# Optimization experiments

Measured on AMD Instinct MI355X. Metric: run time of the kernel, lower is better.

The kernel has to match this reference:

```python
import jax, jax.numpy as jnp
import numpy as np

N_ENTITIES = 4096
FEATURE_DIM = 512
CELLS = 39
PAIRS = 8192


def setup_inputs() -> dict:
    key = jax.random.key(0)
    k_emb, k_idx, k_wg, k_wl = jax.random.split(key, 4)
    embedding = jax.random.normal(k_emb, (N_ENTITIES, FEATURE_DIM), dtype=jnp.float32)
    index = jax.random.randint(k_idx, (CELLS, PAIRS, 2), 0, N_ENTITIES, dtype=jnp.int32)
    # kaiming_uniform-style scale for the global bilinear weight
    bound_g = np.sqrt(6.0 / FEATURE_DIM)
    weights_global = jax.random.uniform(k_wg, (FEATURE_DIM, FEATURE_DIM), minval=-bound_g, maxval=bound_g, dtype=jnp.float32)
    # per-cell diagonal scaling vectors (original stores them as [d,1] params)
    weights_local = jax.random.uniform(k_wl, (CELLS, FEATURE_DIM), minval=-bound_g, maxval=bound_g, dtype=jnp.float32)
    return {"embedding": embedding, "index": index,
            "weights_global": weights_global, "weights_local": weights_local}


def reference(embedding, index, weights_global, weights_local):
    # Original per-cell math: einsum('bn,nm,mj,jk,bk->b', A, diag(wl), W, diag(wl), B)
    # diag(wl) @ ... is just elementwise scaling of the gathered embeddings, so:
    #   out[c,p] = sum_{n,k} (A[c,p,n]*wl[c,n]) * W[n,k] * (B[c,p,k]*wl[c,k])
    wl = weights_local[:, None, :]                      # [C,1,d]
    A = embedding[index[..., 0]] * wl                   # [C,P,d]
    B = embedding[index[..., 1]] * wl                   # [C,P,d]
    return jnp.einsum('cpn,nk,cpk->cp', A, weights_global, B)  # [C,P]
```

## Files before the change

### kernel.cpp

```cpp
#include <hip/hip_runtime.h>
#include <stdint.h>

#define NE 4096
#define FD 512
#define NCELLS 39
#define NPAIRS 8192
#define NT (FD / 64)

typedef __attribute__((ext_vector_type(8))) short short8;
typedef __attribute__((ext_vector_type(8))) unsigned short ushort8;
typedef __attribute__((ext_vector_type(4))) float f32x4;
typedef __attribute__((ext_vector_type(4))) unsigned int uint4v;

__device__ __forceinline__ unsigned short f2bf(float f) {
  union { float f; uint32_t u; } v; v.f = f;
  uint32_t u = v.u;
  return (unsigned short)((u + 0x7fffu + ((u >> 16) & 1u)) >> 16);
}
__device__ __forceinline__ float bf2f(unsigned short b) {
  return __uint_as_float(((uint32_t)b) << 16);
}

__device__ __forceinline__ void async16(const void* g, void* l) {
  __builtin_amdgcn_global_load_lds((const __attribute__((address_space(1))) void*)g,
                                   (__attribute__((address_space(3))) void*)l, 16, 0, 0);
}

__global__ __launch_bounds__(256) void conv_e(const float* __restrict__ E,
                                              unsigned short* __restrict__ Ebf) {
  const int i = blockIdx.x * 256 + threadIdx.x;
  const float4 v = ((const float4*)E)[i];
  ushort4 o;
  o.x = f2bf(v.x); o.y = f2bf(v.y); o.z = f2bf(v.z); o.w = f2bf(v.w);
  ((ushort4*)Ebf)[i] = o;
}

__global__ __launch_bounds__(256) void prep_w(const float* __restrict__ W,
                                              const float* __restrict__ wl,
                                              unsigned short* __restrict__ Wt,
                                              int c0) {
  __shared__ float tile[32][33];
  const int ci = blockIdx.z;
  const int tn = blockIdx.x * 32, tk = blockIdx.y * 32;
  const int tx = threadIdx.x & 31, ty = threadIdx.x >> 5;
  const float* wlr = wl + (size_t)(c0 + ci) * FD;
#pragma unroll
  for (int i = 0; i < 4; i++) {
    int n = tn + ty + i * 8;
    tile[ty + i * 8][tx] = W[(size_t)n * FD + tk + tx] * wlr[n];
  }
  __syncthreads();
  unsigned short* dst = Wt + (size_t)ci * FD * FD;
#pragma unroll
  for (int i = 0; i < 4; i++) {
    int kout = tk + ty + i * 8;
    dst[(size_t)kout * FD + tn + tx] = f2bf(tile[tx][ty + i * 8] * wlr[kout]);
  }
}

__global__ __launch_bounds__(512, 2) void gemm_k(const unsigned short* __restrict__ Ebf,
                                                 const unsigned short* __restrict__ Wt,
                                                 unsigned short* __restrict__ U) {
  __shared__ unsigned short lds[2][2][2][128 * 64];
  const int t = threadIdx.x;
  const int id = blockIdx.x;
  const int xcd = id & 7;
  const int j = id >> 3;
  const int bxh = j & 1;
  const int by = (j >> 1) & 1;
  const int ci = j >> 2;
  const int bx = xcd * 2 + bxh;

  const unsigned short* Ag = Ebf + (size_t)bx * 256 * FD;
  const unsigned short* Bg = Wt + (size_t)ci * FD * FD + (size_t)by * 256 * FD;

  const int wave = t >> 6, lane = t & 63;
  const int wm = wave >> 2, wn = wave & 3;
  const int lr = lane & 15, lq = lane >> 4;

  const int pg0 = t, pg1 = 512 + t;
  const int sr0 = pg0 >> 3, sg0 = pg0 & 7;
  const int sr1 = pg1 >> 3, sg1 = pg1 & 7;
  const int soff0 = sr0 * FD + ((sg0 ^ (sr0 & 7)) << 3);
  const int soff1 = sr1 * FD + ((sg1 ^ (sr1 & 7)) << 3);
  const int loff0 = pg0 * 8, loff1 = pg1 * 8;

  const int swz0 = (lq ^ (lr & 7)) << 3;
  const int swz1 = ((4 + lq) ^ (lr & 7)) << 3;

#define STAGE(OP, HALF, KT, GBASE)                                                \
  do {                                                                            \
    const int bi_ = (KT) & 1;                       \
    const int kt_ = (KT) < NT ? (KT) : (NT - 1);       \
    const unsigned short* gb_ = (GBASE) + (size_t)(HALF) * (128 * FD) + kt_ * 64; \
    unsigned short* d_ = &lds[bi_][OP][HALF][0];                                  \
    async16(gb_ + soff0, d_ + loff0);                                             \
    async16(gb_ + soff1, d_ + loff1);                                             \
  } while (0)

  short8 a[8], b01[4], b23[4];
  f32x4 acc[8][4];
#pragma unroll
  for (int i = 0; i < 8; i++)
#pragma unroll
    for (int j2 = 0; j2 < 4; j2++) acc[i][j2] = (f32x4){0.f, 0.f, 0.f, 0.f};

#define LDA(BUF, MSET)                                                  \
  do {                                                                  \
    const unsigned short* p_ = &lds[BUF][0][wm][0];                     \
    _Pragma("unroll") for (int mi_ = 0; mi_ < 4; ++mi_) {               \
      const int row_ = (MSET) * 64 + mi_ * 16 + lr;                     \
      a[mi_ * 2 + 0] = *(const short8*)&p_[row_ * 64 + swz0];           \
      a[mi_ * 2 + 1] = *(const short8*)&p_[row_ * 64 + swz1];           \
    }                                                                   \
  } while (0)

#define LDB(BUF, NSET, DST)                                             \
  do {                                                                  \
    const unsigned short* p_ = &lds[BUF][1][wn >> 1][0];                \
    _Pragma("unroll") for (int ni_ = 0; ni_ < 2; ++ni_) {               \
      const int row_ = (wn & 1) * 64 + ((NSET) * 2 + ni_) * 16 + lr;    \
      (DST)[ni_ * 2 + 0] = *(const short8*)&p_[row_ * 64 + swz0];       \
      (DST)[ni_ * 2 + 1] = *(const short8*)&p_[row_ * 64 + swz1];       \
    }                                                                   \
  } while (0)

#define MMA(MSET, NSET, B)                                                               \
  do {                                                                                   \
    __builtin_amdgcn_s_setprio(1);                                                       \
    _Pragma("unroll") for (int mi_ = 0; mi_ < 4; ++mi_)                                  \
    _Pragma("unroll") for (int ni_ = 0; ni_ < 2; ++ni_)                                  \
    _Pragma("unroll") for (int s_ = 0; s_ < 2; ++s_)                                     \
      acc[(MSET) * 4 + mi_][(NSET) * 2 + ni_] = __builtin_amdgcn_mfma_f32_16x16x32_bf16( \
          a[mi_ * 2 + s_], (B)[ni_ * 2 + s_],                                            \
          acc[(MSET) * 4 + mi_][(NSET) * 2 + ni_], 0, 0, 0);                             \
    __builtin_amdgcn_s_setprio(0);                                                       \
  } while (0)

#define SYNC_LG()                                        \
  do {                                                   \
    __builtin_amdgcn_s_barrier();                        \
    asm volatile("s_waitcnt lgkmcnt(0)" ::: "memory");   \
  } while (0)

  STAGE(1, 0, 0, Bg); STAGE(0, 0, 0, Ag); STAGE(1, 1, 0, Bg); STAGE(0, 1, 0, Ag);
  STAGE(1, 0, 1, Bg); STAGE(0, 0, 1, Ag);
  asm volatile("s_waitcnt vmcnt(4)" ::: "memory");
  __builtin_amdgcn_s_barrier();

  for (int it = 0; it < NT / 2; ++it) {
    const int k1 = 2 * it + 1, k2 = 2 * it + 2, k3 = 2 * it + 3;
    LDA(0, 0); LDB(0, 0, b01);
    STAGE(1, 1, k1, Bg);
    SYNC_LG(); MMA(0, 0, b01); __builtin_amdgcn_s_barrier();
    LDB(0, 1, b23);
    STAGE(0, 1, k1, Ag);
    SYNC_LG(); MMA(0, 1, b23); __builtin_amdgcn_s_barrier();
    LDA(0, 1);
    STAGE(1, 0, k2, Bg);
    SYNC_LG(); MMA(1, 1, b23); __builtin_amdgcn_s_barrier();
    STAGE(0, 0, k2, Ag);
    __builtin_amdgcn_s_barrier();
    MMA(1, 0, b01);
    asm volatile("s_waitcnt vmcnt(4)" ::: "memory");
    __builtin_amdgcn_s_barrier();
    LDA(1, 0); LDB(1, 0, b01);
    STAGE(1, 1, k2, Bg);
    SYNC_LG(); MMA(0, 0, b01); __builtin_amdgcn_s_barrier();
    LDB(1, 1, b23);
    STAGE(0, 1, k2, Ag);
    SYNC_LG(); MMA(0, 1, b23); __builtin_amdgcn_s_barrier();
    LDA(1, 1);
    STAGE(1, 0, k3, Bg);
    SYNC_LG(); MMA(1, 1, b23); __builtin_amdgcn_s_barrier();
    STAGE(0, 0, k3, Ag);
    __builtin_amdgcn_s_barrier();
    MMA(1, 0, b01);
    asm volatile("s_waitcnt vmcnt(4)" ::: "memory");
    __builtin_amdgcn_s_barrier();
  }

  unsigned short* Up = U + (size_t)ci * NE * FD;
  const int mrow0 = bx * 256 + wm * 128;
  const int ncol0 = by * 256 + wn * 64;
#pragma unroll
  for (int mi = 0; mi < 8; ++mi) {
    const int mbase = mrow0 + mi * 16 + lq * 4;
#pragma unroll
    for (int ni = 0; ni < 4; ++ni) {
      const int n = ncol0 + ni * 16 + lr;
#pragma unroll
      for (int r = 0; r < 4; ++r)
        Up[(size_t)(mbase + r) * FD + n] = f2bf(acc[mi][ni][r]);
    }
  }
#undef STAGE
#undef LDA
#undef LDB
#undef MMA
#undef SYNC_LG
}

__global__ __launch_bounds__(256) void dot_k(const unsigned short* __restrict__ U,
                                             const unsigned short* __restrict__ Ebf,
                                             const int* __restrict__ index,
                                             float* __restrict__ out,
                                             int c0) {
  const int ci = blockIdx.y;
  const int c = c0 + ci;
  const int wave = threadIdx.x >> 6, lane = threadIdx.x & 63;
  const unsigned short* Uc = U + (size_t)ci * NE * FD;
  const size_t cp = (size_t)c * NPAIRS;
  const int2* idx2 = (const int2*)index + cp;
  float* op = out + cp;
  const int pbase = (blockIdx.x * 4 + wave) * 32;

  const int b1 = lane & 1, b2 = (lane >> 1) & 1, b4 = (lane >> 2) & 1;

  for (int batch = 0; batch < 4; batch++) {
    const int pb = pbase + batch * 8;
    int2 id[8];
#pragma unroll
    for (int b = 0; b < 8; b++) id[b] = idx2[pb + b];
    uint4v uv[8], ev[8];
#pragma unroll
    for (int b = 0; b < 8; b++) {
      uv[b] = *(const uint4v*)(Uc + (size_t)id[b].x * FD + lane * 8);
      ev[b] = *(const uint4v*)(Ebf + (size_t)id[b].y * FD + lane * 8);
    }
    float v[8];
#pragma unroll
    for (int b = 0; b < 8; b++) {
      const ushort8 u = *(const ushort8*)&uv[b];
      const ushort8 e = *(const ushort8*)&ev[b];
      float s = 0.f;
#pragma unroll
      for (int q = 0; q < 8; q++) s += bf2f(u[q]) * bf2f(e[q]);
      v[b] = s;
    }
    float w[4];
#pragma unroll
    for (int q = 0; q < 4; q++) {
      const float keep = b1 ? v[2 * q + 1] : v[2 * q];
      const float send = b1 ? v[2 * q] : v[2 * q + 1];
      w[q] = keep + __shfl_xor(send, 1, 64);
    }
    float u2[2];
#pragma unroll
    for (int q = 0; q < 2; q++) {
      const float keep = b2 ? w[2 * q + 1] : w[2 * q];
      const float send = b2 ? w[2 * q] : w[2 * q + 1];
      u2[q] = keep + __shfl_xor(send, 2, 64);
    }
    float f;
    {
      const float keep = b4 ? u2[1] : u2[0];
      const float send = b4 ? u2[0] : u2[1];
      f = keep + __shfl_xor(send, 4, 64);
    }
    f += __shfl_xor(f, 8, 64);
    f += __shfl_xor(f, 16, 64);
    f += __shfl_xor(f, 32, 64);
    if (lane < 8) op[pb + lane] = f;
  }
}

__global__ __launch_bounds__(256) void naive_k(const float* __restrict__ emb,
                                               const int* __restrict__ index,
                                               const float* __restrict__ W,
                                               const float* __restrict__ wl,
                                               float* __restrict__ out) {
  __shared__ float bs[FD];
  __shared__ float red[256];
  const int c = blockIdx.y, p = blockIdx.x;
  const int i0 = index[((size_t)c * NPAIRS + p) * 2];
  const int i1 = index[((size_t)c * NPAIRS + p) * 2 + 1];
  const float* wlc = wl + (size_t)c * FD;
  for (int k = threadIdx.x; k < FD; k += 256) bs[k] = emb[(size_t)i1 * FD + k] * wlc[k];
  __syncthreads();
  float s = 0.f;
  for (int n = threadIdx.x; n < FD; n += 256) {
    const float* wr = W + (size_t)n * FD;
    float tacc = 0.f;
    for (int k = 0; k < FD; k++) tacc += wr[k] * bs[k];
    s += tacc * emb[(size_t)i0 * FD + n] * wlc[n];
  }
  red[threadIdx.x] = s;
  __syncthreads();
  for (int st = 128; st > 0; st >>= 1) {
    if (threadIdx.x < st) red[threadIdx.x] += red[threadIdx.x + st];
    __syncthreads();
  }
  if (threadIdx.x == 0) out[(size_t)c * NPAIRS + p] = red[0];
}

extern "C" void kernel_launch(void* const* d_in, const int* in_sizes, int n_in,
                              void* d_out, int out_size, void* d_ws, size_t ws_size,
                              hipStream_t stream) {
  const float* emb = (const float*)d_in[0];
  const int* index = (const int*)d_in[1];
  const float* Wg = (const float*)d_in[2];
  const float* wl = (const float*)d_in[3];
  float* out = (float*)d_out;

  const size_t ebytes = (size_t)NE * FD * 2;
  const size_t wtcell = (size_t)FD * FD * 2;
  const size_t ucell = (size_t)NE * FD * 2;
  size_t avail = ws_size > ebytes ? ws_size - ebytes : 0;
  int G = (int)(avail / (wtcell + ucell));
  if (G > NCELLS) G = NCELLS;

  if (G < 1) {
    naive_k<<<dim3(NPAIRS, NCELLS), 256, 0, stream>>>(emb, index, Wg, wl, out);
    return;
  }

  unsigned short* Ebf = (unsigned short*)d_ws;
  unsigned short* Wt = (unsigned short*)((char*)d_ws + ebytes);
  unsigned short* U = (unsigned short*)((char*)d_ws + ebytes + (size_t)G * wtcell);

  conv_e<<<dim3((NE * FD / 4) / 256), 256, 0, stream>>>(emb, Ebf);
  for (int c0 = 0; c0 < NCELLS; c0 += G) {
    int g = (NCELLS - c0 < G) ? (NCELLS - c0) : G;
    prep_w<<<dim3(FD / 32, FD / 32, g), 256, 0, stream>>>(Wg, wl, Wt, c0);
    gemm_k<<<dim3(32 * g), 512, 0, stream>>>(Ebf, Wt, U);
    dot_k<<<dim3(NPAIRS / 128, g), 256, 0, stream>>>(U, Ebf, index, out, c0);
  }
}
```

Before: 240.5 us.

## Add persistent GEMM kernel looping over cells with cross-cell prefetch

Adds a persistent GEMM variant launched with 256 blocks. Each block keeps a fixed 256x256 tile of the embedding rows and loops over the cells assigned to its XCD, prefetching the next cell's weight tile into the pipeline while it finishes the current one. The goal is to cut the tail effect of launching 32*39 blocks and to keep the embedding tile hot in cache and LDS addressing. The cost is uneven work per XCD (39 cells over 8 XCDs gives 5 or 4 steps), so some blocks idle at the end. The old chunked path stays as a fallback when the workspace cannot hold every cell.

```diff
diff --git a/kernel.cpp b/kernel.cpp
--- a/kernel.cpp
+++ b/kernel.cpp
@@ -58,7 +58,167 @@
   }
 }
 
-__global__ __launch_bounds__(512, 2) void gemm_k(const unsigned short* __restrict__ Ebf,
+__global__ __launch_bounds__(512, 2) void gemm_p(const unsigned short* __restrict__ Ebf,
+                                                 const unsigned short* __restrict__ Wt,
+                                                 unsigned short* __restrict__ U) {
+  __shared__ unsigned short lds[2][2][2][128 * 64];
+  const int t = threadIdx.x;
+  const int id = blockIdx.x;
+  const int xcd = id & 7;
+  const int cu = id >> 3;
+  const int bx = cu >> 1;
+  const int by = cu & 1;
+  const int nsteps = (NCELLS + 7 - xcd) >> 3;
+
+  const unsigned short* Ag = Ebf + (size_t)bx * 256 * FD;
+
+  const int wave = t >> 6, lane = t & 63;
+  const int wm = wave >> 2, wn = wave & 3;
+  const int lr = lane & 15, lq = lane >> 4;
+
+  const int pg0 = t, pg1 = 512 + t;
+  const int sr0 = pg0 >> 3, sg0 = pg0 & 7;
+  const int sr1 = pg1 >> 3, sg1 = pg1 & 7;
+  const int soff0 = sr0 * FD + ((sg0 ^ (sr0 & 7)) << 3);
+  const int soff1 = sr1 * FD + ((sg1 ^ (sr1 & 7)) << 3);
+  const int loff0 = pg0 * 8, loff1 = pg1 * 8;
+
+  const int swz0 = (lq ^ (lr & 7)) << 3;
+  const int swz1 = ((4 + lq) ^ (lr & 7)) << 3;
+
+#define STAGEP(OP, HALF, KT, CURB, NXTB)                                          \
+  do {                                                                            \
+    const int ktv_ = (KT);                                                        \
+    const int bi_ = ktv_ & 1;                                                     \
+    const unsigned short* base_ = (ktv_ < NT) ? (CURB) : (NXTB);                  \
+    const int kt_ = ktv_ & (NT - 1);                                              \
+    const unsigned short* gb_ = base_ + (size_t)(HALF) * (128 * FD) + kt_ * 64;   \
+    unsigned short* d_ = &lds[bi_][OP][HALF][0];                                  \
+    async16(gb_ + soff0, d_ + loff0);                                             \
+    async16(gb_ + soff1, d_ + loff1);                                             \
+  } while (0)
+
+  short8 a[8], b01[4], b23[4];
+  f32x4 acc[8][4];
+#pragma unroll
+  for (int i = 0; i < 8; i++)
+#pragma unroll
+    for (int j2 = 0; j2 < 4; j2++) acc[i][j2] = (f32x4){0.f, 0.f, 0.f, 0.f};
+
+#define LDAP(BUF, MSET)                                                 \
+  do {                                                                  \
+    const unsigned short* p_ = &lds[BUF][0][wm][0];                     \
+    _Pragma("unroll") for (int mi_ = 0; mi_ < 4; ++mi_) {               \
+      const int row_ = (MSET) * 64 + mi_ * 16 + lr;                     \
+      a[mi_ * 2 + 0] = *(const short8*)&p_[row_ * 64 + swz0];           \
+      a[mi_ * 2 + 1] = *(const short8*)&p_[row_ * 64 + swz1];           \
+    }                                                                   \
+  } while (0)
+
+#define LDBP(BUF, NSET, DST)                                            \
+  do {                                                                  \
+    const unsigned short* p_ = &lds[BUF][1][wn >> 1][0];                \
+    _Pragma("unroll") for (int ni_ = 0; ni_ < 2; ++ni_) {               \
+      const int row_ = (wn & 1) * 64 + ((NSET) * 2 + ni_) * 16 + lr;    \
+      (DST)[ni_ * 2 + 0] = *(const short8*)&p_[row_ * 64 + swz0];       \
+      (DST)[ni_ * 2 + 1] = *(const short8*)&p_[row_ * 64 + swz1];       \
+    }                                                                   \
+  } while (0)
+
+#define MMAP(MSET, NSET, B)                                                              \
+  do {                                                                                   \
+    __builtin_amdgcn_s_setprio(1);                                                       \
+    _Pragma("unroll") for (int mi_ = 0; mi_ < 4; ++mi_)                                  \
+    _Pragma("unroll") for (int ni_ = 0; ni_ < 2; ++ni_)                                  \
+    _Pragma("unroll") for (int s_ = 0; s_ < 2; ++s_)                                     \
+      acc[(MSET) * 4 + mi_][(NSET) * 2 + ni_] = __builtin_amdgcn_mfma_f32_16x16x32_bf16( \
+          a[mi_ * 2 + s_], (B)[ni_ * 2 + s_],                                            \
+          acc[(MSET) * 4 + mi_][(NSET) * 2 + ni_], 0, 0, 0);                             \
+    __builtin_amdgcn_s_setprio(0);                                                       \
+  } while (0)
+
+#define SYNC_LGP()                                       \
+  do {                                                   \
+    __builtin_amdgcn_s_barrier();                        \
+    asm volatile("s_waitcnt lgkmcnt(0)" ::: "memory");   \
+  } while (0)
+
+  int ci = xcd;
+  const unsigned short* Bc = Wt + (size_t)ci * FD * FD + (size_t)by * 256 * FD;
+
+  STAGEP(1, 0, 0, Bc, Bc); STAGEP(0, 0, 0, Ag, Ag);
+  STAGEP(1, 1, 0, Bc, Bc); STAGEP(0, 1, 0, Ag, Ag);
+  STAGEP(1, 0, 1, Bc, Bc); STAGEP(0, 0, 1, Ag, Ag);
+  asm volatile("s_waitcnt vmcnt(4)" ::: "memory");
+  __builtin_amdgcn_s_barrier();
+
+  for (int step = 0; step < nsteps; ++step) {
+    const unsigned short* Bn = (step + 1 < nsteps)
+        ? Wt + (size_t)(ci + 8) * FD * FD + (size_t)by * 256 * FD
+        : Bc;
+
+    for (int it = 0; it < NT / 2; ++it) {
+      const int k1 = 2 * it + 1, k2 = 2 * it + 2, k3 = 2 * it + 3;
+      LDAP(0, 0); LDBP(0, 0, b01);
+      STAGEP(1, 1, k1, Bc, Bn);
+      SYNC_LGP(); MMAP(0, 0, b01); __builtin_amdgcn_s_barrier();
+      LDBP(0, 1, b23);
+      STAGEP(0, 1, k1, Ag, Ag);
+      SYNC_LGP(); MMAP(0, 1, b23); __builtin_amdgcn_s_barrier();
+      LDAP(0, 1);
+      STAGEP(1, 0, k2, Bc, Bn);
+      SYNC_LGP(); MMAP(1, 1, b23); __builtin_amdgcn_s_barrier();
+      STAGEP(0, 0, k2, Ag, Ag);
+      __builtin_amdgcn_s_barrier();
+      MMAP(1, 0, b01);
+      asm volatile("s_waitcnt vmcnt(4)" ::: "memory");
+      __builtin_amdgcn_s_barrier();
+      LDAP(1, 0); LDBP(1, 0, b01);
+      STAGEP(1, 1, k2, Bc, Bn);
+      SYNC_LGP(); MMAP(0, 0, b01); __builtin_amdgcn_s_barrier();
+      LDBP(1, 1, b23);
+      STAGEP(0, 1, k2, Ag, Ag);
+      SYNC_LGP(); MMAP(0, 1, b23); __builtin_amdgcn_s_barrier();
+      LDAP(1, 1);
+      STAGEP(1, 0, k3, Bc, Bn);
+      SYNC_LGP(); MMAP(1, 1, b23); __builtin_amdgcn_s_barrier();
+      STAGEP(0, 0, k3, Ag, Ag);
+      __builtin_amdgcn_s_barrier();
+      MMAP(1, 0, b01);
+      asm volatile("s_waitcnt vmcnt(4)" ::: "memory");
+      __builtin_amdgcn_s_barrier();
+    }
+
+    unsigned short* Up = U + (size_t)ci * NE * FD;
+    const int mrow0 = bx * 256 + wm * 128;
+    const int ncol0 = by * 256 + wn * 64;
+#pragma unroll
+    for (int mi = 0; mi < 8; ++mi) {
+      const int mbase = mrow0 + mi * 16 + lq * 4;
+#pragma unroll
+      for (int ni = 0; ni < 4; ++ni) {
+        const int n = ncol0 + ni * 16 + lr;
+#pragma unroll
+        for (int r = 0; r < 4; ++r)
+          Up[(size_t)(mbase + r) * FD + n] = f2bf(acc[mi][ni][r]);
+      }
+    }
+#pragma unroll
+    for (int i = 0; i < 8; i++)
+#pragma unroll
+      for (int j2 = 0; j2 < 4; j2++) acc[i][j2] = (f32x4){0.f, 0.f, 0.f, 0.f};
+
+    ci += 8;
+    Bc = Bn;
+  }
+#undef STAGEP
+#undef LDAP
+#undef LDBP
+#undef MMAP
+#undef SYNC_LGP
+}
+
+__global__ __launch_bounds__(512, 2) void gemm_c(const unsigned short* __restrict__ Ebf,
                                                  const unsigned short* __restrict__ Wt,
                                                  unsigned short* __restrict__ U) {
   __shared__ unsigned short lds[2][2][2][128 * 64];
@@ -66,10 +226,9 @@
   const int id = blockIdx.x;
   const int xcd = id & 7;
   const int j = id >> 3;
-  const int bxh = j & 1;
+  const int bx = xcd * 2 + (j & 1);
   const int by = (j >> 1) & 1;
   const int ci = j >> 2;
-  const int bx = xcd * 2 + bxh;
 
   const unsigned short* Ag = Ebf + (size_t)bx * 256 * FD;
   const unsigned short* Bg = Wt + (size_t)ci * FD * FD + (size_t)by * 256 * FD;
@@ -84,14 +243,13 @@
   const int soff0 = sr0 * FD + ((sg0 ^ (sr0 & 7)) << 3);
   const int soff1 = sr1 * FD + ((sg1 ^ (sr1 & 7)) << 3);
   const int loff0 = pg0 * 8, loff1 = pg1 * 8;
-
   const int swz0 = (lq ^ (lr & 7)) << 3;
   const int swz1 = ((4 + lq) ^ (lr & 7)) << 3;
 
 #define STAGE(OP, HALF, KT, GBASE)                                                \
   do {                                                                            \
-    const int bi_ = (KT) & 1;                       \
-    const int kt_ = (KT) < NT ? (KT) : (NT - 1);       \
+    const int bi_ = (KT) & 1;                                                     \
+    const int kt_ = (KT) < NT ? (KT) : (NT - 1);                                  \
     const unsigned short* gb_ = (GBASE) + (size_t)(HALF) * (128 * FD) + kt_ * 64; \
     unsigned short* d_ = &lds[bi_][OP][HALF][0];                                  \
     async16(gb_ + soff0, d_ + loff0);                                             \
@@ -320,10 +478,18 @@
   unsigned short* U = (unsigned short*)((char*)d_ws + ebytes + (size_t)G * wtcell);
 
   conv_e<<<dim3((NE * FD / 4) / 256), 256, 0, stream>>>(emb, Ebf);
+
+  if (G >= NCELLS) {
+    prep_w<<<dim3(FD / 32, FD / 32, NCELLS), 256, 0, stream>>>(Wg, wl, Wt, 0);
+    gemm_p<<<dim3(256), 512, 0, stream>>>(Ebf, Wt, U);
+    dot_k<<<dim3(NPAIRS / 128, NCELLS), 256, 0, stream>>>(U, Ebf, index, out, 0);
+    return;
+  }
+
   for (int c0 = 0; c0 < NCELLS; c0 += G) {
     int g = (NCELLS - c0 < G) ? (NCELLS - c0) : G;
     prep_w<<<dim3(FD / 32, FD / 32, g), 256, 0, stream>>>(Wg, wl, Wt, c0);
-    gemm_k<<<dim3(32 * g), 512, 0, stream>>>(Ebf, Wt, U);
+    gemm_c<<<dim3(32 * g), 512, 0, stream>>>(Ebf, Wt, U);
     dot_k<<<dim3(NPAIRS / 128, g), 256, 0, stream>>>(U, Ebf, index, out, c0);
   }
 }
```

New measurement: 299.0 us. 1.24x slower.

## Fuse pair dot products into GEMM epilogue via LDS-resident U tiles

Applied to the files above, without the earlier changes.

The GEMM's bf16 U tile is no longer written to global memory. It is kept in LDS, and each block scans the cell's index list, queuing the pairs whose first entity falls in its 256-row block. It then computes half-dot products against the matching 256-column slice of E and writes them to a partial buffer, which a small kernel sums over the two column halves. This removes the global U write and the gather-read traffic, and launches all cells at once. In exchange, every block scans all 8192 indices, uses an LDS atomic queue, and may see load imbalance.

```diff
diff --git a/kernel.cpp b/kernel.cpp
--- a/kernel.cpp
+++ b/kernel.cpp
@@ -58,18 +58,21 @@
   }
 }
 
-__global__ __launch_bounds__(512, 2) void gemm_k(const unsigned short* __restrict__ Ebf,
+__global__ __launch_bounds__(512, 2) void gemm_f(const unsigned short* __restrict__ Ebf,
                                                  const unsigned short* __restrict__ Wt,
-                                                 unsigned short* __restrict__ U) {
+                                                 const int* __restrict__ index,
+                                                 float* __restrict__ partial) {
   __shared__ unsigned short lds[2][2][2][128 * 64];
+  __shared__ int2 queue[2048];
+  __shared__ int qcnt;
+
   const int t = threadIdx.x;
   const int id = blockIdx.x;
   const int xcd = id & 7;
   const int j = id >> 3;
-  const int bxh = j & 1;
+  const int bx = xcd * 2 + (j & 1);
   const int by = (j >> 1) & 1;
   const int ci = j >> 2;
-  const int bx = xcd * 2 + bxh;
 
   const unsigned short* Ag = Ebf + (size_t)bx * 256 * FD;
   const unsigned short* Bg = Wt + (size_t)ci * FD * FD + (size_t)by * 256 * FD;
@@ -90,8 +93,8 @@
 
 #define STAGE(OP, HALF, KT, GBASE)                                                \
   do {                                                                            \
-    const int bi_ = (KT) & 1;                       \
-    const int kt_ = (KT) < NT ? (KT) : (NT - 1);       \
+    const int bi_ = (KT) & 1;                                                     \
+    const int kt_ = (KT) < NT ? (KT) : (NT - 1);                                  \
     const unsigned short* gb_ = (GBASE) + (size_t)(HALF) * (128 * FD) + kt_ * 64; \
     unsigned short* d_ = &lds[bi_][OP][HALF][0];                                  \
     async16(gb_ + soff0, d_ + loff0);                                             \
@@ -180,19 +183,91 @@
     __builtin_amdgcn_s_barrier();
   }
 
-  unsigned short* Up = U + (size_t)ci * NE * FD;
-  const int mrow0 = bx * 256 + wm * 128;
-  const int ncol0 = by * 256 + wn * 64;
-#pragma unroll
-  for (int mi = 0; mi < 8; ++mi) {
-    const int mbase = mrow0 + mi * 16 + lq * 4;
-#pragma unroll
-    for (int ni = 0; ni < 4; ++ni) {
-      const int n = ncol0 + ni * 16 + lr;
-#pragma unroll
-      for (int r = 0; r < 4; ++r)
-        Up[(size_t)(mbase + r) * FD + n] = f2bf(acc[mi][ni][r]);
+  asm volatile("s_waitcnt vmcnt(0)" ::: "memory");
+  __syncthreads();
+
+  unsigned short* Ut = &lds[0][0][0][0];
+  {
+    const int mrow0w = wm * 128, ncol0w = wn * 64;
+#pragma unroll
+    for (int mi = 0; mi < 8; ++mi)
+#pragma unroll
+      for (int ni = 0; ni < 4; ++ni)
+#pragma unroll
+        for (int r = 0; r < 4; ++r) {
+          const int row = mrow0w + mi * 16 + lq * 4 + r;
+          const int col = ncol0w + ni * 16 + lr;
+          Ut[row * 256 + (col ^ ((row & 12) << 2))] = f2bf(acc[mi][ni][r]);
+        }
+  }
+  __syncthreads();
+
+  const int2* idxc = (const int2*)index + (size_t)ci * NPAIRS;
+  const unsigned short* Eslice = Ebf + by * 256;
+  float* pc = partial + ((size_t)by * NCELLS + ci) * NPAIRS;
+  const int b1 = lane & 1, b2 = (lane >> 1) & 1, b4 = (lane >> 2) & 1;
+
+  for (int seg = 0; seg < NPAIRS; seg += 2048) {
+    if (t == 0) qcnt = 0;
+    __syncthreads();
+#pragma unroll
+    for (int k2 = 0; k2 < 4; ++k2) {
+      const int e = seg + t + k2 * 512;
+      const int2 ie = idxc[e];
+      if ((ie.x >> 8) == bx) {
+        const int pos = atomicAdd(&qcnt, 1);
+        queue[pos] = make_int2(e, (ie.y << 8) | (ie.x & 255));
+      }
     }
+    __syncthreads();
+    const int cnt = qcnt;
+    for (int base = wave * 8; base < cnt; base += 64) {
+      float v[8];
+#pragma unroll
+      for (int jj = 0; jj < 8; ++jj) {
+        float s = 0.f;
+        const int item = base + jj;
+        if (item < cnt) {
+          const int2 qe = queue[item];
+          const int i0l = qe.y & 255;
+          const int i1 = qe.y >> 8;
+          const ushort4 uu =
+              *(const ushort4*)&Ut[i0l * 256 + ((lane * 4) ^ ((i0l & 12) << 2))];
+          const ushort4 ee = *(const ushort4*)&Eslice[(size_t)i1 * FD + lane * 4];
+          s = bf2f(uu.x) * bf2f(ee.x) + bf2f(uu.y) * bf2f(ee.y) +
+              bf2f(uu.z) * bf2f(ee.z) + bf2f(uu.w) * bf2f(ee.w);
+        }
+        v[jj] = s;
+      }
+      float w[4];
+#pragma unroll
+      for (int q = 0; q < 4; ++q) {
+        const float keep = b1 ? v[2 * q + 1] : v[2 * q];
+        const float send = b1 ? v[2 * q] : v[2 * q + 1];
+        w[q] = keep + __shfl_xor(send, 1, 64);
+      }
+      float u2[2];
+#pragma unroll
+      for (int q = 0; q < 2; ++q) {
+        const float keep = b2 ? w[2 * q + 1] : w[2 * q];
+        const float send = b2 ? w[2 * q] : w[2 * q + 1];
+        u2[q] = keep + __shfl_xor(send, 2, 64);
+      }
+      float f;
+      {
+        const float keep = b4 ? u2[1] : u2[0];
+        const float send = b4 ? u2[0] : u2[1];
+        f = keep + __shfl_xor(send, 4, 64);
+      }
+      f += __shfl_xor(f, 8, 64);
+      f += __shfl_xor(f, 16, 64);
+      f += __shfl_xor(f, 32, 64);
+      if (lane < 8 && base + lane < cnt) {
+        const int p = queue[base + lane].x;
+        pc[p] = f;
+      }
+    }
+    __syncthreads();
   }
 #undef STAGE
 #undef LDA
@@ -201,68 +276,10 @@
 #undef SYNC_LG
 }
 
-__global__ __launch_bounds__(256) void dot_k(const unsigned short* __restrict__ U,
-                                             const unsigned short* __restrict__ Ebf,
-                                             const int* __restrict__ index,
-                                             float* __restrict__ out,
-                                             int c0) {
-  const int ci = blockIdx.y;
-  const int c = c0 + ci;
-  const int wave = threadIdx.x >> 6, lane = threadIdx.x & 63;
-  const unsigned short* Uc = U + (size_t)ci * NE * FD;
-  const size_t cp = (size_t)c * NPAIRS;
-  const int2* idx2 = (const int2*)index + cp;
-  float* op = out + cp;
-  const int pbase = (blockIdx.x * 4 + wave) * 32;
-
-  const int b1 = lane & 1, b2 = (lane >> 1) & 1, b4 = (lane >> 2) & 1;
-
-  for (int batch = 0; batch < 4; batch++) {
-    const int pb = pbase + batch * 8;
-    int2 id[8];
-#pragma unroll
-    for (int b = 0; b < 8; b++) id[b] = idx2[pb + b];
-    uint4v uv[8], ev[8];
-#pragma unroll
-    for (int b = 0; b < 8; b++) {
-      uv[b] = *(const uint4v*)(Uc + (size_t)id[b].x * FD + lane * 8);
-      ev[b] = *(const uint4v*)(Ebf + (size_t)id[b].y * FD + lane * 8);
-    }
-    float v[8];
-#pragma unroll
-    for (int b = 0; b < 8; b++) {
-      const ushort8 u = *(const ushort8*)&uv[b];
-      const ushort8 e = *(const ushort8*)&ev[b];
-      float s = 0.f;
-#pragma unroll
-      for (int q = 0; q < 8; q++) s += bf2f(u[q]) * bf2f(e[q]);
-      v[b] = s;
-    }
-    float w[4];
-#pragma unroll
-    for (int q = 0; q < 4; q++) {
-      const float keep = b1 ? v[2 * q + 1] : v[2 * q];
-      const float send = b1 ? v[2 * q] : v[2 * q + 1];
-      w[q] = keep + __shfl_xor(send, 1, 64);
-    }
-    float u2[2];
-#pragma unroll
-    for (int q = 0; q < 2; q++) {
-      const float keep = b2 ? w[2 * q + 1] : w[2 * q];
-      const float send = b2 ? w[2 * q] : w[2 * q + 1];
-      u2[q] = keep + __shfl_xor(send, 2, 64);
-    }
-    float f;
-    {
-      const float keep = b4 ? u2[1] : u2[0];
-      const float send = b4 ? u2[0] : u2[1];
-      f = keep + __shfl_xor(send, 4, 64);
-    }
-    f += __shfl_xor(f, 8, 64);
-    f += __shfl_xor(f, 16, 64);
-    f += __shfl_xor(f, 32, 64);
-    if (lane < 8) op[pb + lane] = f;
-  }
+__global__ __launch_bounds__(256) void comb_k(const float* __restrict__ partial,
+                                              float* __restrict__ out) {
+  const int i = blockIdx.x * 256 + threadIdx.x;
+  out[i] = partial[i] + partial[(size_t)NCELLS * NPAIRS + i];
 }
 
 __global__ __launch_bounds__(256) void naive_k(const float* __restrict__ emb,
@@ -304,26 +321,19 @@
   float* out = (float*)d_out;
 
   const size_t ebytes = (size_t)NE * FD * 2;
-  const size_t wtcell = (size_t)FD * FD * 2;
-  const size_t ucell = (size_t)NE * FD * 2;
-  size_t avail = ws_size > ebytes ? ws_size - ebytes : 0;
-  int G = (int)(avail / (wtcell + ucell));
-  if (G > NCELLS) G = NCELLS;
-
-  if (G < 1) {
+  const size_t wtbytes = (size_t)NCELLS * FD * FD * 2;
+  const size_t pbytes = (size_t)2 * NCELLS * NPAIRS * 4;
+  if (ws_size < ebytes + wtbytes + pbytes) {
     naive_k<<<dim3(NPAIRS, NCELLS), 256, 0, stream>>>(emb, index, Wg, wl, out);
     return;
   }
 
   unsigned short* Ebf = (unsigned short*)d_ws;
   unsigned short* Wt = (unsigned short*)((char*)d_ws + ebytes);
-  unsigned short* U = (unsigned short*)((char*)d_ws + ebytes + (size_t)G * wtcell);
+  float* partial = (float*)((char*)d_ws + ebytes + wtbytes);
 
   conv_e<<<dim3((NE * FD / 4) / 256), 256, 0, stream>>>(emb, Ebf);
-  for (int c0 = 0; c0 < NCELLS; c0 += G) {
-    int g = (NCELLS - c0 < G) ? (NCELLS - c0) : G;
-    prep_w<<<dim3(FD / 32, FD / 32, g), 256, 0, stream>>>(Wg, wl, Wt, c0);
-    gemm_k<<<dim3(32 * g), 512, 0, stream>>>(Ebf, Wt, U);
-    dot_k<<<dim3(NPAIRS / 128, g), 256, 0, stream>>>(U, Ebf, index, out, c0);
-  }
-}
+  prep_w<<<dim3(FD / 32, FD / 32, NCELLS), 256, 0, stream>>>(Wg, wl, Wt, 0);
+  gemm_f<<<dim3(4 * NCELLS * 8), 512, 0, stream>>>(Ebf, Wt, index, partial);
+  comb_k<<<dim3(NCELLS * NPAIRS / 256), 256, 0, stream>>>(partial, out);
+}
```

Measured after the change: 305.8 us. 27.2% more time.
